# Performance work log

Measured on AMD Instinct MI355X. Metric: run time of the kernel, lower is better.

## Reference

```python
import jax, jax.numpy as jnp
import numpy as np

LN_EPS = 1e-5

def _layernorm(x, g, b):
    mu = jnp.mean(x, axis=-1, keepdims=True)
    var = jnp.var(x, axis=-1, keepdims=True)
    return (x - mu) * jax.lax.rsqrt(var + LN_EPS) * g + b

def setup_inputs() -> dict:
    key = jax.random.key(0)
    ks = jax.random.split(key, 8)
    B, T, V, H = 32, 128, 204, 128
    s = 0.02
    x = jax.random.normal(ks[0], (B, T, V, 1), dtype=jnp.float32)
    return {
        "x": x,
        # batched per-variable GRN params
        "fc1_w": jax.random.normal(ks[1], (V, H), dtype=jnp.float32) * s,
        "fc1_b": jnp.zeros((V, H), jnp.float32),
        "fc2_w": jax.random.normal(ks[2], (V, H, H), dtype=jnp.float32) * s,
        "fc2_b": jnp.zeros((V, H), jnp.float32),
        "glu_w": jax.random.normal(ks[3], (V, 2 * H, H), dtype=jnp.float32) * s,
        "glu_b": jnp.zeros((V, 2 * H), jnp.float32),
        "skip_w": jax.random.normal(ks[4], (V, H), dtype=jnp.float32) * s,
        "skip_b": jnp.zeros((V, H), jnp.float32),
        "ln_g": jnp.ones((H,), jnp.float32),
        "ln_b": jnp.zeros((H,), jnp.float32),
        # weight GRN params (input_dim=V, hidden=H, output_dim=V; identity skip)
        "wfc1_w": jax.random.normal(ks[5], (V, H), dtype=jnp.float32) * s,
        "wfc1_b": jnp.zeros((H,), jnp.float32),
        "wfc2_w": jax.random.normal(ks[6], (H, H), dtype=jnp.float32) * s,
        "wfc2_b": jnp.zeros((H,), jnp.float32),
        "wglu_w": jax.random.normal(ks[7], (H, 2 * V), dtype=jnp.float32) * s,
        "wglu_b": jnp.zeros((2 * V,), jnp.float32),
        "wln_g": jnp.ones((V,), jnp.float32),
        "wln_b": jnp.zeros((V,), jnp.float32),
    }

def reference(x, fc1_w, fc1_b, fc2_w, fc2_b, glu_w, glu_b, skip_w, skip_b, ln_g, ln_b,
              wfc1_w, wfc1_b, wfc2_w, wfc2_b, wglu_w, wglu_b, wln_g, wln_b):
    B, T, V, D = x.shape
    H = fc1_w.shape[1]
    xs = x.reshape(B * T, V)  # (N, V) since D == 1

    # --- batched per-variable GRN (eval mode: dropout is identity) ---
    h = jax.nn.elu(xs[..., None] * fc1_w + fc1_b)              # (N, V, H)
    h = jnp.einsum('nvh,vhk->nvk', h, fc2_w) + fc2_b           # bmm over V
    glu = jnp.einsum('nvh,vgh->nvg', h, glu_w) + glu_b         # (N, V, 2H)
    fc_out, gate = glu[..., :H], glu[..., H:]
    h = fc_out * jax.nn.sigmoid(gate)
    skip = xs[..., None] * skip_w + skip_b                     # (N, V, H)
    var_out = _layernorm(skip + h, ln_g, ln_b)                 # (N, V, H)

    # --- weight GRN (input_dim = output_dim = V -> identity skip) ---
    a = jax.nn.elu(xs @ wfc1_w + wfc1_b)                       # (N, H)
    a = a @ wfc2_w + wfc2_b
    g = a @ wglu_w + wglu_b                                    # (N, 2V)
    hg = g[:, :V] * jax.nn.sigmoid(g[:, V:])
    wts = jax.nn.softmax(_layernorm(xs + hg, wln_g, wln_b), axis=-1)  # (N, V)

    out = jnp.einsum('nvh,nv->nh', var_out, wts)               # (N, H)
    return out.reshape(B, T, H), wts.reshape(B, T, V)
```

## Files before the change

### kernel.cpp

```cpp
#include <hip/hip_runtime.h>
#include <hip/hip_bf16.h>

#define NROWS 4096
#define NV    204
#define NH    128
#define NG    256

#define SLOT_B     16384
#define SMS_OFF    (3 * SLOT_B)
#define SMS_BYTES  3584
#define LN_OFF     (SMS_OFF + 2 * SMS_BYTES)
#define LDS_BYTES  (LN_OFF + 1024)

typedef __bf16 bf16x8 __attribute__((ext_vector_type(8)));
typedef float  f32x4  __attribute__((ext_vector_type(4)));

__device__ __forceinline__ float elu_f(float x)  { return x > 0.f ? x : __expf(x) - 1.f; }
__device__ __forceinline__ float sigm_f(float x) { return 1.f / (1.f + __expf(-x)); }

__device__ __forceinline__ void stage16(const void* g, void* l) {
    __builtin_amdgcn_global_load_lds((const __attribute__((address_space(1))) void*)g,
                                     (__attribute__((address_space(3))) void*)l, 16, 0, 0);
}

__device__ __forceinline__ void stage_half(const void* src, char* dst, int w, int l) {
    const char* sb = (const char*)src;
    #pragma unroll
    for (int s = 0; s < 4; ++s)
        stage16(sb + (w * 4 + s) * 1024 + l * 16, dst + (w * 4 + s) * 1024);
}

__device__ __forceinline__ void stage_smalls(const float* src, char* dst, int w, int l) {
    if (w < 3)       stage16((const char*)src + w * 1024 + l * 16, dst + w * 1024);
    else if (l < 32) stage16((const char*)src + 3072 + l * 16,     dst + 3072);
}

#define PSYNC(N) do { \
    asm volatile("s_waitcnt vmcnt(" N ")" ::: "memory"); \
    __builtin_amdgcn_s_barrier(); \
    asm volatile("" ::: "memory"); \
} while (0)

#define NB_FC2 NV
#define NB_GLU (NV * 16)
#define NB_SM  NV
#define NB_WTS (NROWS / 8)

__global__ __launch_bounds__(256) void k_setup(
    const float* __restrict__ fc2_w, __bf16* __restrict__ fc2t,
    const float* __restrict__ glu_w, __bf16* __restrict__ glu16,
    const float* __restrict__ fc1_w, const float* __restrict__ fc1_b,
    const float* __restrict__ fc2_b, const float* __restrict__ glu_b,
    const float* __restrict__ skip_w, const float* __restrict__ skip_b,
    float* __restrict__ smalls,
    const float* __restrict__ xs,
    const float* __restrict__ wfc1_w, const float* __restrict__ wfc1_b,
    const float* __restrict__ wfc2_w, const float* __restrict__ wfc2_b,
    const float* __restrict__ wglu_w, const float* __restrict__ wglu_b,
    const float* __restrict__ wln_g,  const float* __restrict__ wln_b,
    float* __restrict__ wts)
{
    __shared__ float tile[64 * 129];
    __shared__ float sx[8][NV];
    __shared__ float sa[8][NH];
    __shared__ float sg[8][2 * NV];

    const int b = blockIdx.x;
    const int t = threadIdx.x;

    if (b < NB_FC2) {
        const int v = b;
        const float* s = fc2_w + (size_t)v * (NH * NH);
        __bf16*      d = fc2t + (size_t)v * (NH * NH);
        for (int h = 0; h < 2; ++h) {
            __syncthreads();
            for (int i = t; i < 64 * 32; i += 256) {
                const int k = i >> 5, n4 = (i & 31) * 4;
                const float4 f = *(const float4*)(s + (h * 64 + k) * 128 + n4);
                tile[k * 129 + n4 + 0] = f.x;
                tile[k * 129 + n4 + 1] = f.y;
                tile[k * 129 + n4 + 2] = f.z;
                tile[k * 129 + n4 + 3] = f.w;
            }
            __syncthreads();
            for (int i = t; i < 128 * 8; i += 256) {
                const int n = i >> 3, kc = (i & 7) * 8;
                bf16x8 o;
                #pragma unroll
                for (int q = 0; q < 8; ++q) o[q] = (__bf16)tile[(kc + q) * 129 + n];
                const int ch  = h * 8 + (i & 7);
                const int chs = ch ^ (n & 15);
                *(bf16x8*)(d + n * 128 + chs * 8) = o;
            }
        }
        return;
    }

    if (b < NB_FC2 + NB_GLU) {
        const int idx = (b - NB_FC2) * 256 + t;
        const int ch = idx & 15;
        const int g  = (idx >> 4) & 255;
        const int v  = idx >> 12;
        const float* sp = glu_w + (((size_t)v * NG + g) * NH + ch * 8);
        bf16x8 o;
        #pragma unroll
        for (int q = 0; q < 8; ++q) o[q] = (__bf16)sp[q];
        const int dch = ch ^ (g & 15);
        *(bf16x8*)(glu16 + (((size_t)v * NG + g) * NH) + dch * 8) = o;
        return;
    }

    if (b < NB_FC2 + NB_GLU + NB_SM) {
        const int v = b - (NB_FC2 + NB_GLU);
        float* dst = smalls + (size_t)v * 1024;
        for (int idx = t; idx < 896; idx += 256) {
            float val;
            if      (idx < 128)  val = fc1_w[v * NH + idx];
            else if (idx < 256)  val = fc1_b[v * NH + idx - 128];
            else if (idx < 384)  val = fc2_b[v * NH + idx - 256];
            else if (idx < 640)  val = glu_b[v * NG + idx - 384];
            else if (idx < 768)  val = skip_w[v * NH + idx - 640];
            else                 val = skip_b[v * NH + idx - 768];
            dst[idx] = val;
        }
        return;
    }

    const int r0 = (b - NB_FC2 - NB_GLU - NB_SM) * 8;
    const int tr = t >> 5;
    const int tc = t & 31;

    for (int i = t; i < 8 * NV; i += 256) {
        const int r = i / NV, c = i - r * NV;
        sx[r][c] = xs[(size_t)(r0 + r) * NV + c];
    }
    __syncthreads();

    float acc1[4];
    #pragma unroll
    for (int j = 0; j < 4; ++j) acc1[j] = wfc1_b[tc + 32 * j];
    for (int v = 0; v < NV; ++v) {
        const float xv = sx[tr][v];
        #pragma unroll
        for (int j = 0; j < 4; ++j)
            acc1[j] = fmaf(xv, wfc1_w[v * NH + tc + 32 * j], acc1[j]);
    }
    #pragma unroll
    for (int j = 0; j < 4; ++j) sa[tr][tc + 32 * j] = elu_f(acc1[j]);
    __syncthreads();

    float acc2[4];
    #pragma unroll
    for (int j = 0; j < 4; ++j) acc2[j] = wfc2_b[tc + 32 * j];
    for (int h = 0; h < NH; ++h) {
        const float av = sa[tr][h];
        #pragma unroll
        for (int j = 0; j < 4; ++j)
            acc2[j] = fmaf(av, wfc2_w[h * NH + tc + 32 * j], acc2[j]);
    }
    __syncthreads();
    #pragma unroll
    for (int j = 0; j < 4; ++j) sa[tr][tc + 32 * j] = acc2[j];
    __syncthreads();

    float accg[13];
    #pragma unroll
    for (int gi = 0; gi < 12; ++gi) accg[gi] = wglu_b[tc + 32 * gi];
    accg[12] = (tc < 24) ? wglu_b[tc + 384] : 0.f;
    for (int h = 0; h < NH; ++h) {
        const float av = sa[tr][h];
        #pragma unroll
        for (int gi = 0; gi < 12; ++gi)
            accg[gi] = fmaf(av, wglu_w[h * (2 * NV) + tc + 32 * gi], accg[gi]);
        if (tc < 24) accg[12] = fmaf(av, wglu_w[h * (2 * NV) + tc + 384], accg[12]);
    }
    __syncthreads();
    #pragma unroll
    for (int gi = 0; gi < 12; ++gi) sg[tr][tc + 32 * gi] = accg[gi];
    if (tc < 24) sg[tr][tc + 384] = accg[12];
    __syncthreads();

    float tv[7];
    float s1 = 0.f, s2 = 0.f;
    #pragma unroll
    for (int ii = 0; ii < 7; ++ii) {
        const int c = tc + 32 * ii;
        float val = 0.f;
        if (c < NV) {
            const float hg = sg[tr][c] * sigm_f(sg[tr][c + NV]);
            val = sx[tr][c] + hg;
            s1 += val; s2 = fmaf(val, val, s2);
        }
        tv[ii] = val;
    }
    #pragma unroll
    for (int m = 1; m <= 16; m <<= 1) { s1 += __shfl_xor(s1, m); s2 += __shfl_xor(s2, m); }
    const float mu  = s1 * (1.f / 204.f);
    const float var = s2 * (1.f / 204.f) - mu * mu;
    const float rs  = rsqrtf(fmaxf(var, 0.f) + 1e-5f);

    float mx = -1e30f;
    #pragma unroll
    for (int ii = 0; ii < 7; ++ii) {
        const int c = tc + 32 * ii;
        if (c < NV) {
            const float y = fmaf((tv[ii] - mu) * rs, wln_g[c], wln_b[c]);
            tv[ii] = y;
            mx = fmaxf(mx, y);
        }
    }
    #pragma unroll
    for (int m = 1; m <= 16; m <<= 1) mx = fmaxf(mx, __shfl_xor(mx, m));
    float se = 0.f;
    #pragma unroll
    for (int ii = 0; ii < 7; ++ii) {
        const int c = tc + 32 * ii;
        if (c < NV) {
            const float e = __expf(tv[ii] - mx);
            tv[ii] = e;
            se += e;
        }
    }
    #pragma unroll
    for (int m = 1; m <= 16; m <<= 1) se += __shfl_xor(se, m);
    const float inv = 1.f / se;
    #pragma unroll
    for (int ii = 0; ii < 7; ++ii) {
        const int c = tc + 32 * ii;
        if (c < NV) wts[(size_t)(r0 + tr) * NV + c] = tv[ii] * inv;
    }
}

__global__ __launch_bounds__(256, 2) void k_main(
    const float*  __restrict__ xs,
    const __bf16* __restrict__ fc2t,
    const __bf16* __restrict__ glu16,
    const float*  __restrict__ smalls,
    const float*  __restrict__ ln_g,
    const float*  __restrict__ ln_b,
    const float*  __restrict__ wts,
    float*        __restrict__ out)
{
    __shared__ __align__(16) char lds[LDS_BYTES];

    const int tid = threadIdx.x;
    const int w   = tid >> 6;
    const int l   = tid & 63;
    const int l15 = l & 15;
    const int lg  = l >> 4;

    const int vg = blockIdx.x & 7;
    const int m0 = (blockIdx.x >> 3) * 64 + w * 16;
    const int nv = (NV - 1 - vg) / 8 + 1;
    const size_t rowoff = (size_t)(m0 + l15) * NV;

    char* const slot0 = lds;
    char* const slot1 = lds + SLOT_B;
    char* const slot2 = lds + 2 * SLOT_B;

    const f32x4 zero4 = {0.f, 0.f, 0.f, 0.f};
    f32x4 acc_out[8];
    #pragma unroll
    for (int j = 0; j < 8; ++j) acc_out[j] = zero4;

    const int  sh0 = l15 + ((lg & 1) << 5);
    const int  sh1 = sh0 + 16;
    const bool rlo = (lg < 2);

    const float* lnS = (const float*)(lds + LN_OFF);

    float xv, wv, xn, wn;
    {
        if (w == 0) {
            const char* p = (l < 32) ? ((const char*)ln_g + l * 16)
                                     : ((const char*)ln_b + (l - 32) * 16);
            stage16(p, lds + LN_OFF);
        }
        stage_half(fc2t + (size_t)vg * (NH * NH), slot0, w, l);
        stage_smalls(smalls + (size_t)vg * 1024, lds + SMS_OFF, w, l);
        stage_half(fc2t + (size_t)vg * (NH * NH) + 64 * NH, slot1, w, l);
        xv = xs[rowoff + vg];
        wv = wts[rowoff + vg];
    }

    for (int i = 0; i < nv; ++i) {
        const int v  = vg + 8 * i;
        const int vn = (i + 1 < nv) ? v + 8 : v;
        const float* sm = (const float*)(lds + SMS_OFF + (i & 1) * SMS_BYTES);
        const __bf16* gluv = glu16 + (size_t)v * (NG * NH);

        PSYNC("6");
        stage_half(gluv, slot2, w, l);

        bf16x8 a1[4];
        #pragma unroll
        for (int kb = 0; kb < 4; ++kb) {
            const int k0 = kb * 32 + lg * 8;
            const float4 w0 = *(const float4*)(sm + k0);
            const float4 w1 = *(const float4*)(sm + k0 + 4);
            const float4 b0 = *(const float4*)(sm + 128 + k0);
            const float4 b1 = *(const float4*)(sm + 128 + k0 + 4);
            bf16x8 af;
            af[0] = (__bf16)elu_f(fmaf(xv, w0.x, b0.x));
            af[1] = (__bf16)elu_f(fmaf(xv, w0.y, b0.y));
            af[2] = (__bf16)elu_f(fmaf(xv, w0.z, b0.z));
            af[3] = (__bf16)elu_f(fmaf(xv, w0.w, b0.w));
            af[4] = (__bf16)elu_f(fmaf(xv, w1.x, b1.x));
            af[5] = (__bf16)elu_f(fmaf(xv, w1.y, b1.y));
            af[6] = (__bf16)elu_f(fmaf(xv, w1.z, b1.z));
            af[7] = (__bf16)elu_f(fmaf(xv, w1.w, b1.w));
            a1[kb] = af;
        }

        f32x4 h2f[8];
        #pragma unroll
        for (int j = 0; j < 4; ++j) {
            f32x4 acc = zero4;
            const char* rp = slot0 + (j * 16 + l15) * 256;
            #pragma unroll
            for (int kb = 0; kb < 4; ++kb) {
                const bf16x8 wf = *(const bf16x8*)(rp + (((kb * 4 + lg) ^ l15) << 4));
                acc = __builtin_amdgcn_mfma_f32_16x16x32_bf16(wf, a1[kb], acc, 0, 0, 0);
            }
            const float4 fb = *(const float4*)(sm + 256 + j * 16 + lg * 4);
            acc[0] += fb.x; acc[1] += fb.y; acc[2] += fb.z; acc[3] += fb.w;
            h2f[j] = acc;
        }

        PSYNC("6");
        stage_half(gluv + 64 * NH, slot0, w, l);

        #pragma unroll
        for (int j = 4; j < 8; ++j) {
            f32x4 acc = zero4;
            const char* rp = slot1 + ((j - 4) * 16 + l15) * 256;
            #pragma unroll
            for (int kb = 0; kb < 4; ++kb) {
                const bf16x8 wf = *(const bf16x8*)(rp + (((kb * 4 + lg) ^ l15) << 4));
                acc = __builtin_amdgcn_mfma_f32_16x16x32_bf16(wf, a1[kb], acc, 0, 0, 0);
            }
            const float4 fb = *(const float4*)(sm + 256 + j * 16 + lg * 4);
            acc[0] += fb.x; acc[1] += fb.y; acc[2] += fb.z; acc[3] += fb.w;
            h2f[j] = acc;
        }

        bf16x8 b2[4];
        #pragma unroll
        for (int kb2 = 0; kb2 < 4; ++kb2) {
            union U { __bf16 h[4]; int i2[2]; };
            U P, Q;
            P.h[0] = (__bf16)h2f[2 * kb2 + 0][0]; P.h[1] = (__bf16)h2f[2 * kb2 + 0][1];
            P.h[2] = (__bf16)h2f[2 * kb2 + 0][2]; P.h[3] = (__bf16)h2f[2 * kb2 + 0][3];
            Q.h[0] = (__bf16)h2f[2 * kb2 + 1][0]; Q.h[1] = (__bf16)h2f[2 * kb2 + 1][1];
            Q.h[2] = (__bf16)h2f[2 * kb2 + 1][2]; Q.h[3] = (__bf16)h2f[2 * kb2 + 1][3];
            const int px0 = __shfl(P.i2[0], sh0), qx0 = __shfl(Q.i2[0], sh0);
            const int py0 = __shfl(P.i2[1], sh0), qy0 = __shfl(Q.i2[1], sh0);
            const int px1 = __shfl(P.i2[0], sh1), qx1 = __shfl(Q.i2[0], sh1);
            const int py1 = __shfl(P.i2[1], sh1), qy1 = __shfl(Q.i2[1], sh1);
            union V { int ii[4]; bf16x8 vv; } R;
            R.ii[0] = rlo ? px0 : qx0;
            R.ii[1] = rlo ? py0 : qy0;
            R.ii[2] = rlo ? px1 : qx1;
            R.ii[3] = rlo ? py1 : qy1;
            b2[kb2] = R.vv;
        }

        PSYNC("4");
        stage_half(gluv + 128 * NH, slot1, w, l);

        f32x4 fco[8];
        #pragma unroll
        for (int j = 0; j < 4; ++j) {
            f32x4 acc = zero4;
            const char* rp = slot2 + (j * 16 + l15) * 256;
            #pragma unroll
            for (int kb = 0; kb < 4; ++kb) {
                const bf16x8 wf = *(const bf16x8*)(rp + (((kb * 4 + lg) ^ l15) << 4));
                acc = __builtin_amdgcn_mfma_f32_16x16x32_bf16(wf, b2[kb], acc, 0, 0, 0);
            }
            const float4 gb = *(const float4*)(sm + 384 + j * 16 + lg * 4);
            acc[0] += gb.x; acc[1] += gb.y; acc[2] += gb.z; acc[3] += gb.w;
            fco[j] = acc;
        }

        PSYNC("4");
        stage_half(gluv + 192 * NH, slot2, w, l);

        #pragma unroll
        for (int j = 4; j < 8; ++j) {
            f32x4 acc = zero4;
            const char* rp = slot0 + ((j - 4) * 16 + l15) * 256;
            #pragma unroll
            for (int kb = 0; kb < 4; ++kb) {
                const bf16x8 wf = *(const bf16x8*)(rp + (((kb * 4 + lg) ^ l15) << 4));
                acc = __builtin_amdgcn_mfma_f32_16x16x32_bf16(wf, b2[kb], acc, 0, 0, 0);
            }
            const float4 gb = *(const float4*)(sm + 384 + j * 16 + lg * 4);
            acc[0] += gb.x; acc[1] += gb.y; acc[2] += gb.z; acc[3] += gb.w;
            fco[j] = acc;
        }

        PSYNC("4");
        stage_half(fc2t + (size_t)vn * (NH * NH), slot0, w, l);

        f32x4 sv[8];
        #pragma unroll
        for (int j = 0; j < 4; ++j) {
            f32x4 acc = zero4;
            const char* rp = slot1 + (j * 16 + l15) * 256;
            #pragma unroll
            for (int kb = 0; kb < 4; ++kb) {
                const bf16x8 wg = *(const bf16x8*)(rp + (((kb * 4 + lg) ^ l15) << 4));
                acc = __builtin_amdgcn_mfma_f32_16x16x32_bf16(wg, b2[kb], acc, 0, 0, 0);
            }
            const float4 bga = *(const float4*)(sm + 512 + j * 16 + lg * 4);
            const float4 sw4 = *(const float4*)(sm + 640 + j * 16 + lg * 4);
            const float4 sb4 = *(const float4*)(sm + 768 + j * 16 + lg * 4);
            f32x4 s;
            s[0] = fmaf(xv, sw4.x, sb4.x) + fco[j][0] * sigm_f(acc[0] + bga.x);
            s[1] = fmaf(xv, sw4.y, sb4.y) + fco[j][1] * sigm_f(acc[1] + bga.y);
            s[2] = fmaf(xv, sw4.z, sb4.z) + fco[j][2] * sigm_f(acc[2] + bga.z);
            s[3] = fmaf(xv, sw4.w, sb4.w) + fco[j][3] * sigm_f(acc[3] + bga.w);
            sv[j] = s;
        }

        PSYNC("4");
        stage_smalls(smalls + (size_t)vn * 1024,
                     lds + SMS_OFF + ((i + 1) & 1) * SMS_BYTES, w, l);
        stage_half(fc2t + (size_t)vn * (NH * NH) + 64 * NH, slot1, w, l);
        xn = xs[rowoff + vn];
        wn = wts[rowoff + vn];

        #pragma unroll
        for (int j = 4; j < 8; ++j) {
            f32x4 acc = zero4;
            const char* rp = slot2 + ((j - 4) * 16 + l15) * 256;
            #pragma unroll
            for (int kb = 0; kb < 4; ++kb) {
                const bf16x8 wg = *(const bf16x8*)(rp + (((kb * 4 + lg) ^ l15) << 4));
                acc = __builtin_amdgcn_mfma_f32_16x16x32_bf16(wg, b2[kb], acc, 0, 0, 0);
            }
            const float4 bga = *(const float4*)(sm + 512 + j * 16 + lg * 4);
            const float4 sw4 = *(const float4*)(sm + 640 + j * 16 + lg * 4);
            const float4 sb4 = *(const float4*)(sm + 768 + j * 16 + lg * 4);
            f32x4 s;
            s[0] = fmaf(xv, sw4.x, sb4.x) + fco[j][0] * sigm_f(acc[0] + bga.x);
            s[1] = fmaf(xv, sw4.y, sb4.y) + fco[j][1] * sigm_f(acc[1] + bga.y);
            s[2] = fmaf(xv, sw4.z, sb4.z) + fco[j][2] * sigm_f(acc[2] + bga.z);
            s[3] = fmaf(xv, sw4.w, sb4.w) + fco[j][3] * sigm_f(acc[3] + bga.w);
            sv[j] = s;
        }

        float t1 = 0.f, t2 = 0.f;
        #pragma unroll
        for (int j = 0; j < 8; ++j) {
            #pragma unroll
            for (int r = 0; r < 4; ++r) { t1 += sv[j][r]; t2 = fmaf(sv[j][r], sv[j][r], t2); }
        }
        t1 += __shfl_xor(t1, 16); t2 += __shfl_xor(t2, 16);
        t1 += __shfl_xor(t1, 32); t2 += __shfl_xor(t2, 32);
        const float mu  = t1 * (1.f / 128.f);
        const float var = t2 * (1.f / 128.f) - mu * mu;
        const float rsv = rsqrtf(fmaxf(var, 0.f) + 1e-5f);

        #pragma unroll
        for (int j = 0; j < 8; ++j) {
            const float4 lg4 = *(const float4*)(lnS + j * 16 + lg * 4);
            const float4 lb4 = *(const float4*)(lnS + 128 + j * 16 + lg * 4);
            const float y0 = fmaf((sv[j][0] - mu) * rsv, lg4.x, lb4.x);
            const float y1 = fmaf((sv[j][1] - mu) * rsv, lg4.y, lb4.y);
            const float y2 = fmaf((sv[j][2] - mu) * rsv, lg4.z, lb4.z);
            const float y3 = fmaf((sv[j][3] - mu) * rsv, lg4.w, lb4.w);
            acc_out[j][0] = fmaf(wv, y0, acc_out[j][0]);
            acc_out[j][1] = fmaf(wv, y1, acc_out[j][1]);
            acc_out[j][2] = fmaf(wv, y2, acc_out[j][2]);
            acc_out[j][3] = fmaf(wv, y3, acc_out[j][3]);
        }

        xv = xn; wv = wn;
    }

    asm volatile("s_waitcnt vmcnt(0)" ::: "memory");

    #pragma unroll
    for (int j = 0; j < 8; ++j) {
        #pragma unroll
        for (int r = 0; r < 4; ++r)
            atomicAdd(&out[(size_t)(m0 + l15) * NH + j * 16 + lg * 4 + r], acc_out[j][r]);
    }
}

extern "C" void kernel_launch(void* const* d_in, const int* in_sizes, int n_in,
                              void* d_out, int out_size, void* d_ws, size_t ws_size,
                              hipStream_t stream) {
    (void)in_sizes; (void)n_in; (void)out_size; (void)ws_size;

    const float* xs     = (const float*)d_in[0];
    const float* fc1_w  = (const float*)d_in[1];
    const float* fc1_b  = (const float*)d_in[2];
    const float* fc2_w  = (const float*)d_in[3];
    const float* fc2_b  = (const float*)d_in[4];
    const float* glu_w  = (const float*)d_in[5];
    const float* glu_b  = (const float*)d_in[6];
    const float* skip_w = (const float*)d_in[7];
    const float* skip_b = (const float*)d_in[8];
    const float* ln_g   = (const float*)d_in[9];
    const float* ln_b   = (const float*)d_in[10];
    const float* wfc1_w = (const float*)d_in[11];
    const float* wfc1_b = (const float*)d_in[12];
    const float* wfc2_w = (const float*)d_in[13];
    const float* wfc2_b = (const float*)d_in[14];
    const float* wglu_w = (const float*)d_in[15];
    const float* wglu_b = (const float*)d_in[16];
    const float* wln_g  = (const float*)d_in[17];
    const float* wln_b  = (const float*)d_in[18];

    float* out = (float*)d_out;
    float* wts = out + (size_t)NROWS * NH;

    __bf16* fc2t   = (__bf16*)d_ws;
    __bf16* glu16  = fc2t + (size_t)NV * NH * NH;
    float*  smalls = (float*)(glu16 + (size_t)NV * NG * NH);

    hipMemsetAsync(d_out, 0, (size_t)NROWS * NH * sizeof(float), stream);

    k_setup<<<NB_FC2 + NB_GLU + NB_SM + NB_WTS, 256, 0, stream>>>(
        fc2_w, fc2t, glu_w, glu16,
        fc1_w, fc1_b, fc2_b, glu_b, skip_w, skip_b, smalls,
        xs, wfc1_w, wfc1_b, wfc2_w, wfc2_b, wglu_w, wglu_b, wln_g, wln_b, wts);

    k_main<<<(NROWS / 64) * 8, 256, 0, stream>>>(xs, fc2t, glu16, smalls,
                                                 ln_g, ln_b, wts, out);
}
```

Before: 330.7 us.

## Seed MFMA accumulators with biases, single-buffer smalls, add wave priority hints

The MFMA accumulators now start from the bias vectors loaded from LDS, so the separate bias adds after each GEMM tile are gone. The double-buffered per-variable smalls region becomes one buffer, refilled after an added block-wide barrier at the end of each iteration. The PSYNC wait counts are retuned to match. s_setprio raises wave priority around the MFMA sections, and the glu weight conversion now uses float4 loads. The new barrier and single buffer can serialize the smalls load with the next iteration's start in exchange for a smaller LDS footprint.

```diff
diff --git a/kernel.cpp b/kernel.cpp
--- a/kernel.cpp
+++ b/kernel.cpp
@@ -9,7 +9,7 @@
 #define SLOT_B     16384
 #define SMS_OFF    (3 * SLOT_B)
 #define SMS_BYTES  3584
-#define LN_OFF     (SMS_OFF + 2 * SMS_BYTES)
+#define LN_OFF     (SMS_OFF + SMS_BYTES)
 #define LDS_BYTES  (LN_OFF + 1024)
 
 typedef __bf16 bf16x8 __attribute__((ext_vector_type(8)));
@@ -102,9 +102,11 @@
         const int g  = (idx >> 4) & 255;
         const int v  = idx >> 12;
         const float* sp = glu_w + (((size_t)v * NG + g) * NH + ch * 8);
+        const float4 f0 = *(const float4*)(sp);
+        const float4 f1 = *(const float4*)(sp + 4);
         bf16x8 o;
-        #pragma unroll
-        for (int q = 0; q < 8; ++q) o[q] = (__bf16)sp[q];
+        o[0] = (__bf16)f0.x; o[1] = (__bf16)f0.y; o[2] = (__bf16)f0.z; o[3] = (__bf16)f0.w;
+        o[4] = (__bf16)f1.x; o[5] = (__bf16)f1.y; o[6] = (__bf16)f1.z; o[7] = (__bf16)f1.w;
         const int dch = ch ^ (g & 15);
         *(bf16x8*)(glu16 + (((size_t)v * NG + g) * NH) + dch * 8) = o;
         return;
@@ -267,6 +269,7 @@
     const int  sh1 = sh0 + 16;
     const bool rlo = (lg < 2);
 
+    const float* sm  = (const float*)(lds + SMS_OFF);
     const float* lnS = (const float*)(lds + LN_OFF);
 
     float xv, wv, xn, wn;
@@ -277,8 +280,8 @@
             stage16(p, lds + LN_OFF);
         }
         stage_half(fc2t + (size_t)vg * (NH * NH), slot0, w, l);
+        stage_half(fc2t + (size_t)vg * (NH * NH) + 64 * NH, slot1, w, l);
         stage_smalls(smalls + (size_t)vg * 1024, lds + SMS_OFF, w, l);
-        stage_half(fc2t + (size_t)vg * (NH * NH) + 64 * NH, slot1, w, l);
         xv = xs[rowoff + vg];
         wv = wts[rowoff + vg];
     }
@@ -286,10 +289,9 @@
     for (int i = 0; i < nv; ++i) {
         const int v  = vg + 8 * i;
         const int vn = (i + 1 < nv) ? v + 8 : v;
-        const float* sm = (const float*)(lds + SMS_OFF + (i & 1) * SMS_BYTES);
         const __bf16* gluv = glu16 + (size_t)v * (NG * NH);
 
-        PSYNC("6");
+        PSYNC("0");
         stage_half(gluv, slot2, w, l);
 
         bf16x8 a1[4];
@@ -313,36 +315,36 @@
         }
 
         f32x4 h2f[8];
+        __builtin_amdgcn_s_setprio(1);
         #pragma unroll
         for (int j = 0; j < 4; ++j) {
-            f32x4 acc = zero4;
+            f32x4 acc = *(const f32x4*)(sm + 256 + j * 16 + lg * 4);
             const char* rp = slot0 + (j * 16 + l15) * 256;
             #pragma unroll
             for (int kb = 0; kb < 4; ++kb) {
                 const bf16x8 wf = *(const bf16x8*)(rp + (((kb * 4 + lg) ^ l15) << 4));
                 acc = __builtin_amdgcn_mfma_f32_16x16x32_bf16(wf, a1[kb], acc, 0, 0, 0);
             }
-            const float4 fb = *(const float4*)(sm + 256 + j * 16 + lg * 4);
-            acc[0] += fb.x; acc[1] += fb.y; acc[2] += fb.z; acc[3] += fb.w;
             h2f[j] = acc;
         }
-
-        PSYNC("6");
+        __builtin_amdgcn_s_setprio(0);
+
+        PSYNC("4");
         stage_half(gluv + 64 * NH, slot0, w, l);
 
+        __builtin_amdgcn_s_setprio(1);
         #pragma unroll
         for (int j = 4; j < 8; ++j) {
-            f32x4 acc = zero4;
+            f32x4 acc = *(const f32x4*)(sm + 256 + j * 16 + lg * 4);
             const char* rp = slot1 + ((j - 4) * 16 + l15) * 256;
             #pragma unroll
             for (int kb = 0; kb < 4; ++kb) {
                 const bf16x8 wf = *(const bf16x8*)(rp + (((kb * 4 + lg) ^ l15) << 4));
                 acc = __builtin_amdgcn_mfma_f32_16x16x32_bf16(wf, a1[kb], acc, 0, 0, 0);
             }
-            const float4 fb = *(const float4*)(sm + 256 + j * 16 + lg * 4);
-            acc[0] += fb.x; acc[1] += fb.y; acc[2] += fb.z; acc[3] += fb.w;
             h2f[j] = acc;
         }
+        __builtin_amdgcn_s_setprio(0);
 
         bf16x8 b2[4];
         #pragma unroll
@@ -369,87 +371,94 @@
         stage_half(gluv + 128 * NH, slot1, w, l);
 
         f32x4 fco[8];
+        __builtin_amdgcn_s_setprio(1);
         #pragma unroll
         for (int j = 0; j < 4; ++j) {
-            f32x4 acc = zero4;
+            f32x4 acc = *(const f32x4*)(sm + 384 + j * 16 + lg * 4);
             const char* rp = slot2 + (j * 16 + l15) * 256;
             #pragma unroll
             for (int kb = 0; kb < 4; ++kb) {
                 const bf16x8 wf = *(const bf16x8*)(rp + (((kb * 4 + lg) ^ l15) << 4));
                 acc = __builtin_amdgcn_mfma_f32_16x16x32_bf16(wf, b2[kb], acc, 0, 0, 0);
             }
-            const float4 gb = *(const float4*)(sm + 384 + j * 16 + lg * 4);
-            acc[0] += gb.x; acc[1] += gb.y; acc[2] += gb.z; acc[3] += gb.w;
             fco[j] = acc;
         }
+        __builtin_amdgcn_s_setprio(0);
 
         PSYNC("4");
         stage_half(gluv + 192 * NH, slot2, w, l);
 
+        __builtin_amdgcn_s_setprio(1);
         #pragma unroll
         for (int j = 4; j < 8; ++j) {
-            f32x4 acc = zero4;
+            f32x4 acc = *(const f32x4*)(sm + 384 + j * 16 + lg * 4);
             const char* rp = slot0 + ((j - 4) * 16 + l15) * 256;
             #pragma unroll
             for (int kb = 0; kb < 4; ++kb) {
                 const bf16x8 wf = *(const bf16x8*)(rp + (((kb * 4 + lg) ^ l15) << 4));
                 acc = __builtin_amdgcn_mfma_f32_16x16x32_bf16(wf, b2[kb], acc, 0, 0, 0);
             }
-            const float4 gb = *(const float4*)(sm + 384 + j * 16 + lg * 4);
-            acc[0] += gb.x; acc[1] += gb.y; acc[2] += gb.z; acc[3] += gb.w;
             fco[j] = acc;
         }
+        __builtin_amdgcn_s_setprio(0);
 
         PSYNC("4");
         stage_half(fc2t + (size_t)vn * (NH * NH), slot0, w, l);
 
         f32x4 sv[8];
+        __builtin_amdgcn_s_setprio(1);
         #pragma unroll
         for (int j = 0; j < 4; ++j) {
-            f32x4 acc = zero4;
+            f32x4 acc = *(const f32x4*)(sm + 512 + j * 16 + lg * 4);
             const char* rp = slot1 + (j * 16 + l15) * 256;
             #pragma unroll
             for (int kb = 0; kb < 4; ++kb) {
                 const bf16x8 wg = *(const bf16x8*)(rp + (((kb * 4 + lg) ^ l15) << 4));
                 acc = __builtin_amdgcn_mfma_f32_16x16x32_bf16(wg, b2[kb], acc, 0, 0, 0);
             }
-            const float4 bga = *(const float4*)(sm + 512 + j * 16 + lg * 4);
+            __builtin_amdgcn_s_setprio(0);
             const float4 sw4 = *(const float4*)(sm + 640 + j * 16 + lg * 4);
             const float4 sb4 = *(const float4*)(sm + 768 + j * 16 + lg * 4);
             f32x4 s;
-            s[0] = fmaf(xv, sw4.x, sb4.x) + fco[j][0] * sigm_f(acc[0] + bga.x);
-            s[1] = fmaf(xv, sw4.y, sb4.y) + fco[j][1] * sigm_f(acc[1] + bga.y);
-            s[2] = fmaf(xv, sw4.z, sb4.z) + fco[j][2] * sigm_f(acc[2] + bga.z);
-            s[3] = fmaf(xv, sw4.w, sb4.w) + fco[j][3] * sigm_f(acc[3] + bga.w);
+            s[0] = fmaf(xv, sw4.x, sb4.x) + fco[j][0] * sigm_f(acc[0]);
+            s[1] = fmaf(xv, sw4.y, sb4.y) + fco[j][1] * sigm_f(acc[1]);
+            s[2] = fmaf(xv, sw4.z, sb4.z) + fco[j][2] * sigm_f(acc[2]);
+            s[3] = fmaf(xv, sw4.w, sb4.w) + fco[j][3] * sigm_f(acc[3]);
             sv[j] = s;
-        }
+            __builtin_amdgcn_s_setprio(1);
+        }
+        __builtin_amdgcn_s_setprio(0);
 
         PSYNC("4");
-        stage_smalls(smalls + (size_t)vn * 1024,
-                     lds + SMS_OFF + ((i + 1) & 1) * SMS_BYTES, w, l);
         stage_half(fc2t + (size_t)vn * (NH * NH) + 64 * NH, slot1, w, l);
         xn = xs[rowoff + vn];
         wn = wts[rowoff + vn];
 
+        __builtin_amdgcn_s_setprio(1);
         #pragma unroll
         for (int j = 4; j < 8; ++j) {
-            f32x4 acc = zero4;
+            f32x4 acc = *(const f32x4*)(sm + 512 + j * 16 + lg * 4);
             const char* rp = slot2 + ((j - 4) * 16 + l15) * 256;
             #pragma unroll
             for (int kb = 0; kb < 4; ++kb) {
                 const bf16x8 wg = *(const bf16x8*)(rp + (((kb * 4 + lg) ^ l15) << 4));
                 acc = __builtin_amdgcn_mfma_f32_16x16x32_bf16(wg, b2[kb], acc, 0, 0, 0);
             }
-            const float4 bga = *(const float4*)(sm + 512 + j * 16 + lg * 4);
+            __builtin_amdgcn_s_setprio(0);
             const float4 sw4 = *(const float4*)(sm + 640 + j * 16 + lg * 4);
             const float4 sb4 = *(const float4*)(sm + 768 + j * 16 + lg * 4);
             f32x4 s;
-            s[0] = fmaf(xv, sw4.x, sb4.x) + fco[j][0] * sigm_f(acc[0] + bga.x);
-            s[1] = fmaf(xv, sw4.y, sb4.y) + fco[j][1] * sigm_f(acc[1] + bga.y);
-            s[2] = fmaf(xv, sw4.z, sb4.z) + fco[j][2] * sigm_f(acc[2] + bga.z);
-            s[3] = fmaf(xv, sw4.w, sb4.w) + fco[j][3] * sigm_f(acc[3] + bga.w);
+            s[0] = fmaf(xv, sw4.x, sb4.x) + fco[j][0] * sigm_f(acc[0]);
+            s[1] = fmaf(xv, sw4.y, sb4.y) + fco[j][1] * sigm_f(acc[1]);
+            s[2] = fmaf(xv, sw4.z, sb4.z) + fco[j][2] * sigm_f(acc[2]);
+            s[3] = fmaf(xv, sw4.w, sb4.w) + fco[j][3] * sigm_f(acc[3]);
             sv[j] = s;
-        }
+            __builtin_amdgcn_s_setprio(1);
+        }
+        __builtin_amdgcn_s_setprio(0);
+
+        __syncthreads();
+        stage_smalls(smalls + (size_t)vn * 1024, lds + SMS_OFF, w, l);
 
         float t1 = 0.f, t2 = 0.f;
         #pragma unroll
```

New measurement: 337.2 us. No clear change (+2.0%).
